# Kernel optimization log

Measured on AMD Instinct MI355X. Metric: run time of the kernel, lower is better.

Reference implementation:

```python
import jax, jax.numpy as jnp
import numpy as np


def setup_inputs() -> dict:
    key = jax.random.key(0)
    k1, k2, k3, k4, k5 = jax.random.split(key, 5)
    H = W = 128
    C = 256
    N = 2000
    A = 7
    features_map = jax.random.normal(k1, (1, H, W, C), dtype=jnp.float32)
    # valid integer boxes: x2 > x1, y2 > y1, in-bounds
    x1 = jax.random.randint(k2, (N,), 0, W - 8)
    y1 = jax.random.randint(k3, (N,), 0, H - 8)
    bw = jax.random.randint(k4, (N,), 4, 48)
    bh = jax.random.randint(k5, (N,), 4, 48)
    x2 = jnp.minimum(x1 + bw, W)
    y2 = jnp.minimum(y1 + bh, H)
    boxes = jnp.stack([x1, y1, x2, y2], axis=-1).astype(jnp.int32)
    return {"features_map": features_map, "boxes": boxes, "anchor_size": A}


def reference(features_map, boxes, anchor_size):
    # Fused ROI pooling: per box, bilinear-resize the crop [y1:y2, x1:x2]
    # to (anchor_size, anchor_size), matching tf.image.resize bilinear
    # (half-pixel centers, edge clamped inside the crop).
    A = int(anchor_size)
    fm = features_map[0]  # [H, W, C]

    def axis_samples(lo, hi):
        span = (hi - lo).astype(jnp.float32)
        src = (jnp.arange(A, dtype=jnp.float32) + 0.5) * (span / A) - 0.5
        src = jnp.clip(src, 0.0, jnp.maximum(span - 1.0, 0.0))
        i0 = jnp.floor(src).astype(jnp.int32)
        i1 = jnp.minimum(i0 + 1, hi - lo - 1)
        frac = src - i0.astype(jnp.float32)
        return i0 + lo, i1 + lo, frac

    def pool_one(box):
        x1, y1, x2, y2 = box[0], box[1], box[2], box[3]
        ys0, ys1, fy = axis_samples(y1, y2)  # [A]
        xs0, xs1, fx = axis_samples(x1, x2)  # [A]
        v00 = fm[ys0[:, None], xs0[None, :]]  # [A, A, C]
        v01 = fm[ys0[:, None], xs1[None, :]]
        v10 = fm[ys1[:, None], xs0[None, :]]
        v11 = fm[ys1[:, None], xs1[None, :]]
        fy_ = fy[:, None, None]
        fx_ = fx[None, :, None]
        top = v00 * (1.0 - fx_) + v01 * fx_
        bot = v10 * (1.0 - fx_) + v11 * fx_
        return (top * (1.0 - fy_) + bot * fy_)[None]  # [1, A, A, C]

    return jax.vmap(pool_one)(boxes)  # [N, 1, A, A, C]
```

## Files before the change

kernel.cpp:

```cpp
#include <hip/hip_runtime.h>
#include <hip/hip_bf16.h>


#define FM_H 128
#define FM_W 128
#define FM_C 256
#define ANCH 7
#define NSAMP (ANCH * ANCH)

typedef float f4 __attribute__((ext_vector_type(4)));

__global__ __launch_bounds__(256) void sort_boxes_kernel(
    const int* __restrict__ boxes, int* __restrict__ order, int n_boxes)
{
    __shared__ int cursor[64];
    const int tid = threadIdx.x;
    if (tid < 64) cursor[tid] = 0;
    __syncthreads();

    for (int i = tid; i < n_boxes; i += 256) {
        const int x1 = boxes[i * 4 + 0];
        const int y1 = boxes[i * 4 + 1];
        const int key = ((y1 >> 4) << 3) | (x1 >> 4);
        atomicAdd(&cursor[key], 1);
    }
    __syncthreads();

    if (tid == 0) {
        int run = 0;
        for (int k = 0; k < 64; ++k) {
            int c = cursor[k];
            cursor[k] = run;
            run += c;
        }
    }
    __syncthreads();

    for (int i = tid; i < n_boxes; i += 256) {
        const int x1 = boxes[i * 4 + 0];
        const int y1 = boxes[i * 4 + 1];
        const int key = ((y1 >> 4) << 3) | (x1 >> 4);
        const int pos = atomicAdd(&cursor[key], 1);
        order[pos] = i;
    }
}

__global__ __launch_bounds__(256) void roi_pool_kernel(
    const float* __restrict__ fm,
    const int* __restrict__ boxes,
    const int* __restrict__ order,
    float* __restrict__ out,
    int n_samples)
{
    const int nb  = gridDim.x;
    const int b   = blockIdx.x;
    const int q   = nb >> 3;
    const int r   = nb & 7;
    const int xcd = b & 7;
    const int idx = b >> 3;
    const int sb  = (xcd < r ? xcd * (q + 1) : r * (q + 1) + (xcd - r) * q) + idx;

    const int lane = threadIdx.x & 63;
    const int wave = __builtin_amdgcn_readfirstlane((sb << 2) + (threadIdx.x >> 6));
    if (wave >= n_samples) return;

    const int sorted_box = wave / NSAMP;
    const int s   = wave - sorted_box * NSAMP;
    const int py  = s / ANCH;
    const int px  = s - py * ANCH;
    const int box = order[sorted_box];

    const int x1 = boxes[box * 4 + 0];
    const int y1 = boxes[box * 4 + 1];
    const int x2 = boxes[box * 4 + 2];
    const int y2 = boxes[box * 4 + 3];

    const float spany = (float)(y2 - y1);
    float sy = ((float)py + 0.5f) * (spany / (float)ANCH) - 0.5f;
    sy = fminf(fmaxf(sy, 0.0f), fmaxf(spany - 1.0f, 0.0f));
    const int iy0 = (int)floorf(sy);
    const int iy1 = min(iy0 + 1, y2 - y1 - 1);
    const float fy = sy - (float)iy0;
    const int ys0 = iy0 + y1;
    const int ys1 = iy1 + y1;

    const float spanx = (float)(x2 - x1);
    float sx = ((float)px + 0.5f) * (spanx / (float)ANCH) - 0.5f;
    sx = fminf(fmaxf(sx, 0.0f), fmaxf(spanx - 1.0f, 0.0f));
    const int ix0 = (int)floorf(sx);
    const int ix1 = min(ix0 + 1, x2 - x1 - 1);
    const float fx = sx - (float)ix0;
    const int xs0 = ix0 + x1;
    const int xs1 = ix1 + x1;

    const f4* p00 = (const f4*)(fm + ((size_t)ys0 * FM_W + xs0) * FM_C);
    const f4* p01 = (const f4*)(fm + ((size_t)ys0 * FM_W + xs1) * FM_C);
    const f4* p10 = (const f4*)(fm + ((size_t)ys1 * FM_W + xs0) * FM_C);
    const f4* p11 = (const f4*)(fm + ((size_t)ys1 * FM_W + xs1) * FM_C);

    const f4 v00 = p00[lane];
    const f4 v01 = p01[lane];
    const f4 v10 = p10[lane];
    const f4 v11 = p11[lane];

    const float gx = 1.0f - fx;
    const float gy = 1.0f - fy;

    f4 res;
    #pragma unroll
    for (int c = 0; c < 4; ++c) {
        float top = v00[c] * gx + v01[c] * fx;
        float bot = v10[c] * gx + v11[c] * fx;
        res[c] = top * gy + bot * fy;
    }

    f4* dst = (f4*)(out + ((size_t)box * NSAMP + s) * FM_C);
    dst[lane] = res;
}

extern "C" void kernel_launch(void* const* d_in, const int* in_sizes, int n_in,
                              void* d_out, int out_size, void* d_ws, size_t ws_size,
                              hipStream_t stream) {
    const float* fm    = (const float*)d_in[0];
    const int*   boxes = (const int*)d_in[1];

    const int N = in_sizes[1] / 4;
    const int n_samples = N * NSAMP;

    float* out  = (float*)d_out;
    int* order  = (int*)d_ws;

    sort_boxes_kernel<<<1, 256, 0, stream>>>(boxes, order, N);

    const int threads = 256;
    const int waves_per_block = threads / 64;
    const int grid = (n_samples + waves_per_block - 1) / waves_per_block;

    roi_pool_kernel<<<grid, threads, 0, stream>>>(fm, boxes, order, out, n_samples);
}
```

Measured before the change: 35.95 us.

## Convert feature map to fp16 in a fused prep kernel before ROI gather

Adds a prep kernel that converts the fp32 feature map into an fp16 copy in workspace, running alongside the box-sorting block in the same launch. The ROI pooling kernel is templated and reads the fp16 copy, halving the bytes per gathered corner, with non-temporal stores for the output. The conversion reads and writes the whole 16 MB map on every call, which adds memory traffic. It also loses precision relative to the fp32 reference. When workspace is too small it falls back to the fp32 path.

```diff
diff --git a/kernel.cpp b/kernel.cpp
--- a/kernel.cpp
+++ b/kernel.cpp
@@ -1,5 +1,6 @@
 #include <hip/hip_runtime.h>
 #include <hip/hip_bf16.h>
+#include <hip/hip_fp16.h>
 
 
 #define FM_H 128
@@ -7,12 +8,33 @@
 #define FM_C 256
 #define ANCH 7
 #define NSAMP (ANCH * ANCH)
+#define FM_ELEMS (FM_H * FM_W * FM_C)
+#define CONV_BLOCKS 256
 
-typedef float f4 __attribute__((ext_vector_type(4)));
+typedef float   f4 __attribute__((ext_vector_type(4)));
+typedef _Float16 h4 __attribute__((ext_vector_type(4)));
 
-__global__ __launch_bounds__(256) void sort_boxes_kernel(
-    const int* __restrict__ boxes, int* __restrict__ order, int n_boxes)
+__global__ __launch_bounds__(256) void prep_kernel(
+    const float* __restrict__ fm, const int* __restrict__ boxes,
+    _Float16* __restrict__ fm16, int* __restrict__ order,
+    int n_boxes, int conv_blocks)
 {
+    if ((int)blockIdx.x < conv_blocks) {
+        const int tid = blockIdx.x * 256 + threadIdx.x;
+        const f4* src = (const f4*)fm;
+        h4* dst = (h4*)fm16;
+        #pragma unroll
+        for (int k = 0; k < 16; ++k) {
+            const int i = tid + k * 65536;
+            const f4 v = src[i];
+            h4 h;
+            h[0] = (_Float16)v[0]; h[1] = (_Float16)v[1];
+            h[2] = (_Float16)v[2]; h[3] = (_Float16)v[3];
+            dst[i] = h;
+        }
+        return;
+    }
+
     __shared__ int cursor[64];
     const int tid = threadIdx.x;
     if (tid < 64) cursor[tid] = 0;
@@ -28,11 +50,7 @@
 
     if (tid == 0) {
         int run = 0;
-        for (int k = 0; k < 64; ++k) {
-            int c = cursor[k];
-            cursor[k] = run;
-            run += c;
-        }
+        for (int k = 0; k < 64; ++k) { int c = cursor[k]; cursor[k] = run; run += c; }
     }
     __syncthreads();
 
@@ -45,8 +63,9 @@
     }
 }
 
-__global__ __launch_bounds__(256) void roi_pool_kernel(
-    const float* __restrict__ fm,
+template <typename ET, typename V4>
+__global__ __launch_bounds__(256) void roi_pool_kernel_t(
+    const ET* __restrict__ fmx,
     const int* __restrict__ boxes,
     const int* __restrict__ order,
     float* __restrict__ out,
@@ -68,7 +87,7 @@
     const int s   = wave - sorted_box * NSAMP;
     const int py  = s / ANCH;
     const int px  = s - py * ANCH;
-    const int box = order[sorted_box];
+    const int box = order ? order[sorted_box] : sorted_box;
 
     const int x1 = boxes[box * 4 + 0];
     const int y1 = boxes[box * 4 + 1];
@@ -93,15 +112,15 @@
     const int xs0 = ix0 + x1;
     const int xs1 = ix1 + x1;
 
-    const f4* p00 = (const f4*)(fm + ((size_t)ys0 * FM_W + xs0) * FM_C);
-    const f4* p01 = (const f4*)(fm + ((size_t)ys0 * FM_W + xs1) * FM_C);
-    const f4* p10 = (const f4*)(fm + ((size_t)ys1 * FM_W + xs0) * FM_C);
-    const f4* p11 = (const f4*)(fm + ((size_t)ys1 * FM_W + xs1) * FM_C);
+    const V4* p00 = (const V4*)(fmx + ((size_t)(ys0 * FM_W + xs0)) * FM_C);
+    const V4* p01 = (const V4*)(fmx + ((size_t)(ys0 * FM_W + xs1)) * FM_C);
+    const V4* p10 = (const V4*)(fmx + ((size_t)(ys1 * FM_W + xs0)) * FM_C);
+    const V4* p11 = (const V4*)(fmx + ((size_t)(ys1 * FM_W + xs1)) * FM_C);
 
-    const f4 v00 = p00[lane];
-    const f4 v01 = p01[lane];
-    const f4 v10 = p10[lane];
-    const f4 v11 = p11[lane];
+    const V4 v00 = p00[lane];
+    const V4 v01 = p01[lane];
+    const V4 v10 = p10[lane];
+    const V4 v11 = p11[lane];
 
     const float gx = 1.0f - fx;
     const float gy = 1.0f - fy;
@@ -109,13 +128,13 @@
     f4 res;
     #pragma unroll
     for (int c = 0; c < 4; ++c) {
-        float top = v00[c] * gx + v01[c] * fx;
-        float bot = v10[c] * gx + v11[c] * fx;
+        const float top = (float)v00[c] * gx + (float)v01[c] * fx;
+        const float bot = (float)v10[c] * gx + (float)v11[c] * fx;
         res[c] = top * gy + bot * fy;
     }
 
-    f4* dst = (f4*)(out + ((size_t)box * NSAMP + s) * FM_C);
-    dst[lane] = res;
+    f4* dst = (f4*)(out + ((size_t)(box * NSAMP + s)) * FM_C);
+    __builtin_nontemporal_store(res, &dst[lane]);
 }
 
 extern "C" void kernel_launch(void* const* d_in, const int* in_sizes, int n_in,
@@ -126,15 +145,29 @@
 
     const int N = in_sizes[1] / 4;
     const int n_samples = N * NSAMP;
+    float* out = (float*)d_out;
 
-    float* out  = (float*)d_out;
-    int* order  = (int*)d_ws;
-
-    sort_boxes_kernel<<<1, 256, 0, stream>>>(boxes, order, N);
+    const size_t f16_bytes   = (size_t)FM_ELEMS * sizeof(_Float16);
+    const size_t order_bytes = (size_t)N * sizeof(int);
 
     const int threads = 256;
-    const int waves_per_block = threads / 64;
-    const int grid = (n_samples + waves_per_block - 1) / waves_per_block;
+    const int grid = (n_samples + 3) / 4;
 
-    roi_pool_kernel<<<grid, threads, 0, stream>>>(fm, boxes, order, out, n_samples);
+    if (ws_size >= f16_bytes + order_bytes) {
+        _Float16* fm16 = (_Float16*)d_ws;
+        int* order = (int*)((char*)d_ws + f16_bytes);
+
+        prep_kernel<<<CONV_BLOCKS + 1, 256, 0, stream>>>(
+            fm, boxes, fm16, order, N, CONV_BLOCKS);
+        roi_pool_kernel_t<_Float16, h4><<<grid, threads, 0, stream>>>(
+            fm16, boxes, order, out, n_samples);
+    } else if (ws_size >= order_bytes) {
+        int* order = (int*)d_ws;
+        prep_kernel<<<1, 256, 0, stream>>>(fm, boxes, nullptr, order, N, 0);
+        roi_pool_kernel_t<float, f4><<<grid, threads, 0, stream>>>(
+            fm, boxes, order, out, n_samples);
+    } else {
+        roi_pool_kernel_t<float, f4><<<grid, threads, 0, stream>>>(
+            fm, boxes, nullptr, out, n_samples);
+    }
 }
```

After: 34.98 us. 2.7% less time.
